# Kernel tuning notes

Hardware: AMD Instinct MI355X
Metric: run time of the kernel (lower is better)

The kernel has to match this reference:

```python
import jax, jax.numpy as jnp
import numpy as np

N = 500_000
H = 256
G = 4096
NUM_TIMESTEPS = 2


def setup_inputs() -> dict:
    key = jax.random.key(0)
    ks = jax.random.split(key, 12)
    s = 0.05
    x = jax.random.normal(ks[0], (N, H), dtype=jnp.float32)
    batch = jnp.sort(jax.random.randint(ks[1], (N,), 0, G, dtype=jnp.int64))
    return {
        "x": x,
        "gate_w1": jax.random.normal(ks[2], (H, H), dtype=jnp.float32) * s,
        "gate_b1": jax.random.normal(ks[3], (H,), dtype=jnp.float32) * s,
        "gate_w2": jax.random.normal(ks[4], (1, H), dtype=jnp.float32) * s,
        "gate_b2": jax.random.normal(ks[5], (1,), dtype=jnp.float32) * s,
        "gru_w_ih": jax.random.normal(ks[6], (3 * H, H), dtype=jnp.float32) * s,
        "gru_w_hh": jax.random.normal(ks[7], (3 * H, H), dtype=jnp.float32) * s,
        "gru_b_ih": jax.random.normal(ks[8], (3 * H,), dtype=jnp.float32) * s,
        "gru_b_hh": jax.random.normal(ks[9], (3 * H,), dtype=jnp.float32) * s,
        "batch": batch,
        "num_graphs": G,
    }


def _gru_cell(inp, h, w_ih, w_hh, b_ih, b_hh):
    # torch.nn.GRUCell semantics; gate order [r, z, n]
    gi = inp @ w_ih.T + b_ih
    gh = h @ w_hh.T + b_hh
    i_r, i_z, i_n = jnp.split(gi, 3, axis=-1)
    h_r, h_z, h_n = jnp.split(gh, 3, axis=-1)
    r = jax.nn.sigmoid(i_r + h_r)
    z = jax.nn.sigmoid(i_z + h_z)
    n = jnp.tanh(i_n + r * h_n)
    return (1.0 - z) * n + z * h


def reference(x, gate_w1, gate_b1, gate_w2, gate_b2,
              gru_w_ih, gru_w_hh, gru_b_ih, gru_b_hh,
              batch, num_graphs):
    counts = jax.ops.segment_sum(jnp.ones((x.shape[0],), x.dtype), batch,
                                 num_segments=num_graphs)
    denom = jnp.maximum(counts, 1.0)[:, None]  # empty graphs -> 0 mean

    def mean_pool(v):
        return jax.ops.segment_sum(v, batch, num_segments=num_graphs) / denom

    graph_repr = mean_pool(x)  # (G, H)
    for _ in range(NUM_TIMESTEPS):
        # gather per-node graph context (batch is sorted == node_to_graph)
        gate_input = x + graph_repr[batch]  # (N, H)
        hgate = jax.nn.relu(gate_input @ gate_w1.T + gate_b1)
        gate = jax.nn.sigmoid(hgate @ gate_w2.T + gate_b2)  # (N, 1)
        weighted_x = x * gate
        new_graph_repr = mean_pool(weighted_x)
        graph_repr = _gru_cell(new_graph_repr, graph_repr,
                               gru_w_ih, gru_w_hh, gru_b_ih, gru_b_hh)
        graph_repr = jax.nn.relu(graph_repr)
    return graph_repr
```

## Files before the change

### kernel.cpp

```cpp
#include <hip/hip_runtime.h>
#include <hip/hip_bf16.h>
#include <stdint.h>

#define H 256
#define G 4096
#define TK 32
#define TP0 128

typedef __attribute__((ext_vector_type(8))) short bf16x8;
typedef __attribute__((ext_vector_type(4))) float f32x4;

__device__ inline short f2bf(float f){
  union { float f; uint32_t u; } v; v.f = f;
  uint32_t r = (v.u + 0x7FFFu + ((v.u >> 16) & 1u)) >> 16;
  return (short)(uint16_t)r;
}
__device__ inline float bf2f(short s){
  union { float f; uint32_t u; } v; v.u = ((uint32_t)(uint16_t)s) << 16;
  return v.f;
}
__device__ inline uint32_t pk2(float lo, float hi){
  return (uint32_t)(uint16_t)f2bf(lo) | ((uint32_t)(uint16_t)f2bf(hi) << 16);
}
__device__ inline uint32_t pkfp8(float4 v){
  int u = __builtin_amdgcn_cvt_pk_fp8_f32(v.x, v.y, 0, false);
  u = __builtin_amdgcn_cvt_pk_fp8_f32(v.z, v.w, u, true);
  return (uint32_t)u;
}
__device__ inline float sigmoidf_(float x){ return 1.f / (1.f + __expf(-x)); }

__device__ inline void ldsbar(){
  asm volatile("s_waitcnt lgkmcnt(0)" ::: "memory");
  __builtin_amdgcn_s_barrier();
}

__global__ void conv_w(const float* __restrict__ w1, const float* __restrict__ wih,
                       const float* __restrict__ whh,
                       short* __restrict__ o1, short* __restrict__ oih, short* __restrict__ ohh,
                       uint8_t* __restrict__ w1q,
                       float* __restrict__ counts, float* __restrict__ pool){
  int i = blockIdx.x * 256 + threadIdx.x;
  if (i < H*H) o1[i] = f2bf(w1[i]);
  if (i < 3*H*H){ oih[i] = f2bf(wih[i]); ohh[i] = f2bf(whh[i]); }
  if (i < H*H/4){
    float4 v = *(const float4*)(w1 + (size_t)i*4);
    *(uint32_t*)(w1q + (size_t)i*4) = pkfp8(v);
  }
  if (i < G) counts[i] = 0.f;
  for (int j = i; j < G*H; j += 768*256) pool[j] = 0.f;
}

__global__ __launch_bounds__(512) __attribute__((amdgpu_waves_per_eu(2, 8)))
void k0_pool(const float* __restrict__ x, const int* __restrict__ batch,
             float* __restrict__ pool, float* __restrict__ counts,
             short* __restrict__ xbf, uint8_t* __restrict__ xq,
             float* __restrict__ sgate, int nNodes){
  __shared__ int   ng[TP0];
  __shared__ float Pacc[8][H];
  __shared__ float Cacc[8];
  __shared__ int   spanSh;

  const int t = threadIdx.x;
  const int base = blockIdx.x * TP0;
  const int c4 = (t & 63) * 4;
  const int r0 = (t >> 6) * 16;

  float4 v[16];
  #pragma unroll
  for (int i = 0; i < 16; ++i){
    int node = base + r0 + i;
    if (node < nNodes) v[i] = *(const float4*)(x + (size_t)node*H + c4);
    else v[i] = make_float4(0.f,0.f,0.f,0.f);
  }

  { int gi = blockIdx.x * 512 + t; if (gi < nNodes) sgate[gi] = 0.f; }

  if (t < TP0) ng[t] = (base + t < nNodes) ? batch[base + t] : -1;
  for (int u = t; u < 8*H; u += 512) ((float*)Pacc)[u] = 0.f;
  if (t < 8) Cacc[t] = 0.f;
  __syncthreads();

  if (t == 0){
    int lg = ng[0];
    if (base + TP0 <= nNodes) lg = ng[TP0-1];
    else { for (int i = TP0-1; i > 0; --i){ if (ng[i] >= 0){ lg = ng[i]; break; } } }
    spanSh = (ng[0] >= 0) ? (lg - ng[0]) : -1;
  }

  if (xbf){
    #pragma unroll
    for (int i = 0; i < 16; ++i){
      int node = base + r0 + i;
      if (node < nNodes){
        ushort4 o;
        o.x = (uint16_t)f2bf(v[i].x); o.y = (uint16_t)f2bf(v[i].y);
        o.z = (uint16_t)f2bf(v[i].z); o.w = (uint16_t)f2bf(v[i].w);
        *(ushort4*)(xbf + (size_t)node*H + c4) = o;
        *(uint32_t*)(xq + (size_t)node*H + c4) = pkfp8(v[i]);
      }
    }
  }
  __syncthreads();

  const int g0 = ng[0];
  const bool useLds = (spanSh >= 0) && (spanSh < 8);

  float ax=0.f, ay=0.f, az=0.f, aw=0.f;
  int cur = ng[r0];
  if (cur >= 0){
    #pragma unroll
    for (int i = 0; i < 16; ++i){
      int g = ng[r0 + i];
      if (g < 0) break;
      if (g != cur){
        if (useLds){
          atomicAdd(&Pacc[cur-g0][c4], ax);   atomicAdd(&Pacc[cur-g0][c4+1], ay);
          atomicAdd(&Pacc[cur-g0][c4+2], az); atomicAdd(&Pacc[cur-g0][c4+3], aw);
        } else {
          atomicAdd(&pool[(size_t)cur*H + c4], ax);   atomicAdd(&pool[(size_t)cur*H + c4+1], ay);
          atomicAdd(&pool[(size_t)cur*H + c4+2], az); atomicAdd(&pool[(size_t)cur*H + c4+3], aw);
        }
        ax=ay=az=aw=0.f; cur = g;
      }
      ax += v[i].x; ay += v[i].y; az += v[i].z; aw += v[i].w;
    }
    if (useLds){
      atomicAdd(&Pacc[cur-g0][c4], ax);   atomicAdd(&Pacc[cur-g0][c4+1], ay);
      atomicAdd(&Pacc[cur-g0][c4+2], az); atomicAdd(&Pacc[cur-g0][c4+3], aw);
    } else {
      atomicAdd(&pool[(size_t)cur*H + c4], ax);   atomicAdd(&pool[(size_t)cur*H + c4+1], ay);
      atomicAdd(&pool[(size_t)cur*H + c4+2], az); atomicAdd(&pool[(size_t)cur*H + c4+3], aw);
    }
  }
  if (t < TP0 && ng[t] >= 0){
    if (useLds) atomicAdd(&Cacc[ng[t]-g0], 1.f);
    else        atomicAdd(&counts[ng[t]], 1.f);
  }
  __syncthreads();

  if (useLds){
    int nr = spanSh + 1;
    for (int u = t; u < nr*H; u += 512){
      int r = u >> 8, c = u & 255;
      float vv = Pacc[r][c];
      if (vv != 0.f) atomicAdd(&pool[(size_t)(g0+r)*H + c], vv);
    }
    if (t < nr && Cacc[t] != 0.f) atomicAdd(&counts[g0 + t], Cacc[t]);
  }
}

__global__ void k0b_div(const float* __restrict__ pool, const float* __restrict__ counts,
                        float* __restrict__ repr, float* __restrict__ pool_mut){
  size_t i = (size_t)blockIdx.x * 256 + threadIdx.x;
  int g = (int)(i >> 8);
  repr[i] = pool[i] / fmaxf(counts[g], 1.f);
  pool_mut[i] = 0.f;
}

__global__ __launch_bounds__(256) void kT_hg(const float* __restrict__ repr,
    const short* __restrict__ w1bf, const float* __restrict__ b1,
    uint32_t* __restrict__ hgp){
  __shared__ short Ar[16][H + 8];
  const int t    = threadIdx.x;
  const int wid  = t >> 6;
  const int lane = t & 63;
  const int l15  = lane & 15;
  const int l4   = lane >> 4;
  const int g0   = blockIdx.x * 16;

  for (int u = t; u < 16*32; u += 256){
    int row = u >> 5, cg = u & 31;
    int c0 = cg * 8;
    const float4* rp = (const float4*)(repr + (size_t)(g0+row)*H + c0);
    float4 r0 = rp[0], r1 = rp[1];
    bf16x8 o;
    o[0]=f2bf(r0.x); o[1]=f2bf(r0.y); o[2]=f2bf(r0.z); o[3]=f2bf(r0.w);
    o[4]=f2bf(r1.x); o[5]=f2bf(r1.y); o[6]=f2bf(r1.z); o[7]=f2bf(r1.w);
    *(bf16x8*)(&Ar[row][c0]) = o;
  }
  __syncthreads();

  f32x4 acc[4];
  #pragma unroll
  for (int i = 0; i < 4; ++i) acc[i] = (f32x4){0.f,0.f,0.f,0.f};
  #pragma unroll
  for (int kc = 0; kc < 8; ++kc){
    bf16x8 a = *(bf16x8*)(&Ar[l15][kc*32 + l4*8]);
    #pragma unroll
    for (int nt = 0; nt < 4; ++nt){
      int col = wid*64 + nt*16 + l15;
      bf16x8 b = *(const bf16x8*)(w1bf + (size_t)col*H + kc*32 + l4*8);
      acc[nt] = __builtin_amdgcn_mfma_f32_16x16x32_bf16(a, b, acc[nt], 0, 0, 0);
    }
  }
  const float b1v0 = b1[wid*64 + l15];
  const float b1v1 = b1[wid*64 + 16 + l15];
  const float b1v2 = b1[wid*64 + 32 + l15];
  const float b1v3 = b1[wid*64 + 48 + l15];
  #pragma unroll
  for (int j = 0; j < 4; ++j){
    int row = l4*4 + j;
    hgp[(size_t)(g0+row)*128 + wid*32 + l15]      = pk2(acc[0][j]+b1v0, acc[1][j]+b1v1);
    hgp[(size_t)(g0+row)*128 + wid*32 + 16 + l15] = pk2(acc[2][j]+b1v2, acc[3][j]+b1v3);
  }
}

__global__ __launch_bounds__(256) __attribute__((amdgpu_waves_per_eu(4, 6)))
void k1a_fp8(
    const uint8_t* __restrict__ xq, const int* __restrict__ batch,
    const uint32_t* __restrict__ hgp, const uint8_t* __restrict__ w1q,
    const float* __restrict__ w2, float* __restrict__ sgate,
    int nNodes, int nTiles, int nChains){

  __shared__ uint8_t Ain[2][TK][H + 16];
  __shared__ int     ngS[2][TK];

  const int t    = threadIdx.x;
  const int wid  = t >> 6;
  const int lane = t & 63;
  const int l15  = lane & 15;
  const int l4   = lane >> 4;

  const int ch    = blockIdx.x >= nChains;
  const int chain = ch ? blockIdx.x - nChains : blockIdx.x;
  const int colB  = ch*128 + wid*32;
  const int hgcol = ch*64 + wid*16 + l15;

  const int tile0 = (int)(((long long)chain * nTiles) / nChains);
  const int tile1 = (int)(((long long)(chain+1) * nTiles) / nChains);
  if (tile0 >= tile1) return;

  long Bf0[8], Bf1[8];
  {
    const uint8_t* wp0 = w1q + (size_t)(colB + l15)*H + l4*8;
    #pragma unroll
    for (int kc = 0; kc < 8; ++kc){
      Bf0[kc] = *(const long*)(wp0 + kc*32);
      Bf1[kc] = *(const long*)(wp0 + 16*H + kc*32);
    }
  }
  const float w2v0 = w2[colB + l15];
  const float w2v1 = w2[colB + 16 + l15];

  const int srow  = t >> 4;
  const int scolB = (t & 15) * 16;
  uint4 xv0, xv1;
  int ngv = -1;

  auto issueT = [&](int tile){
    int base = tile * TK;
    int n0 = base + srow, n1 = n0 + 16;
    xv0 = (n0 < nNodes) ? *(const uint4*)(xq + (size_t)n0*H + scolB) : make_uint4(0,0,0,0);
    xv1 = (n1 < nNodes) ? *(const uint4*)(xq + (size_t)n1*H + scolB) : make_uint4(0,0,0,0);
    if (t < TK){
      int node = base + t;
      ngv = (node < nNodes) ? batch[node] : -1;
    }
  };
  auto stageT = [&](int buf){
    *(uint4*)(&Ain[buf][srow][scolB])      = xv0;
    *(uint4*)(&Ain[buf][srow + 16][scolB]) = xv1;
    if (t < TK) ngS[buf][t] = ngv;
  };

  issueT(tile0);
  stageT(0);
  if (tile0 + 1 < tile1) issueT(tile0 + 1);

  int cur = 0;
  for (int tile = tile0; tile < tile1; ++tile, cur ^= 1){
    ldsbar();

    int gr[2][4];
    uint32_t hvp[2][4];
    #pragma unroll
    for (int r = 0; r < 2; ++r)
      #pragma unroll
      for (int j = 0; j < 4; ++j){
        int g = ngS[cur][r*16 + l4*4 + j];
        gr[r][j] = g;
        hvp[r][j] = (g >= 0) ? hgp[(size_t)g*128 + hgcol] : 0u;
      }

    f32x4 acc0[2], acc1[2];
    #pragma unroll
    for (int r = 0; r < 2; ++r){ acc0[r] = (f32x4){0.f,0.f,0.f,0.f}; acc1[r] = (f32x4){0.f,0.f,0.f,0.f}; }
    #pragma unroll
    for (int kc = 0; kc < 8; ++kc){
      #pragma unroll
      for (int r = 0; r < 2; ++r){
        long a = *(const long*)(&Ain[cur][r*16 + l15][kc*32 + l4*8]);
        acc0[r] = __builtin_amdgcn_mfma_f32_16x16x32_fp8_fp8(a, Bf0[kc], acc0[r], 0, 0, 0);
        acc1[r] = __builtin_amdgcn_mfma_f32_16x16x32_fp8_fp8(a, Bf1[kc], acc1[r], 0, 0, 0);
      }
    }

    if (tile + 1 < tile1){
      stageT(cur ^ 1);
      if (tile + 2 < tile1) issueT(tile + 2);
    }

    float p[2][4];
    #pragma unroll
    for (int r = 0; r < 2; ++r)
      #pragma unroll
      for (int j = 0; j < 4; ++j){
        float h0 = fmaxf(acc0[r][j] + bf2f((short)(uint16_t)(hvp[r][j] & 0xFFFFu)), 0.f);
        float h1 = fmaxf(acc1[r][j] + bf2f((short)(uint16_t)(hvp[r][j] >> 16)), 0.f);
        p[r][j] = w2v0*h0 + w2v1*h1;
      }
    #pragma unroll
    for (int off = 1; off < 16; off <<= 1){
      #pragma unroll
      for (int r = 0; r < 2; ++r)
        #pragma unroll
        for (int j = 0; j < 4; ++j) p[r][j] += __shfl_xor(p[r][j], off);
    }
    if (l15 == 0){
      int base = tile * TK;
      #pragma unroll
      for (int r = 0; r < 2; ++r)
        #pragma unroll
        for (int j = 0; j < 4; ++j){
          if (gr[r][j] >= 0)
            atomicAdd(&sgate[base + r*16 + l4*4 + j], p[r][j]);
        }
    }
  }
}

template<bool BF>
__global__ __launch_bounds__(512) __attribute__((amdgpu_waves_per_eu(2, 8)))
void k1b_pool(
    const float* __restrict__ xf32, const short* __restrict__ xbf,
    const int* __restrict__ batch, float* __restrict__ sgate,
    const float* __restrict__ b2p, float* __restrict__ pool, int nNodes){

  __shared__ int   ng[TP0];
  __shared__ float gs[TP0];
  __shared__ float Pacc[8][H];
  __shared__ int   spanSh;

  const int t = threadIdx.x;
  const int base = blockIdx.x * TP0;
  const int c4 = (t & 63) * 4;
  const int r0 = (t >> 6) * 16;

  ushort4 u[16];
  float4  vf[16];
  #pragma unroll
  for (int i = 0; i < 16; ++i){
    int node = base + r0 + i;
    if constexpr (BF){
      u[i] = (node < nNodes) ? *(const ushort4*)(xbf + (size_t)node*H + c4)
                             : make_ushort4(0,0,0,0);
    } else {
      vf[i] = (node < nNodes) ? *(const float4*)(xf32 + (size_t)node*H + c4)
                              : make_float4(0.f,0.f,0.f,0.f);
    }
  }

  const float b2v = b2p[0];
  if (t < TP0){
    int node = base + t;
    if (node < nNodes){
      ng[t] = batch[node];
      gs[t] = sigmoidf_(sgate[node] + b2v);
      sgate[node] = 0.f;
    } else { ng[t] = -1; gs[t] = 0.f; }
  }
  for (int w = t; w < 8*H; w += 512) ((float*)Pacc)[w] = 0.f;
  __syncthreads();

  if (t == 0){
    int lg = ng[0];
    if (base + TP0 <= nNodes) lg = ng[TP0-1];
    else { for (int i = TP0-1; i > 0; --i){ if (ng[i] >= 0){ lg = ng[i]; break; } } }
    spanSh = (ng[0] >= 0) ? (lg - ng[0]) : -1;
  }
  __syncthreads();

  const int g0 = ng[0];
  const bool useLds = (spanSh >= 0) && (spanSh < 8);

  float ax=0.f, ay=0.f, az=0.f, aw=0.f;
  int cur = ng[r0];
  if (cur >= 0){
    #pragma unroll
    for (int i = 0; i < 16; ++i){
      int g = ng[r0 + i];
      if (g < 0) break;
      if (g != cur){
        if (useLds){
          atomicAdd(&Pacc[cur-g0][c4], ax);   atomicAdd(&Pacc[cur-g0][c4+1], ay);
          atomicAdd(&Pacc[cur-g0][c4+2], az); atomicAdd(&Pacc[cur-g0][c4+3], aw);
        } else {
          atomicAdd(&pool[(size_t)cur*H + c4], ax);   atomicAdd(&pool[(size_t)cur*H + c4+1], ay);
          atomicAdd(&pool[(size_t)cur*H + c4+2], az); atomicAdd(&pool[(size_t)cur*H + c4+3], aw);
        }
        ax=ay=az=aw=0.f; cur = g;
      }
      float gv = gs[r0 + i];
      if constexpr (BF){
        ax += gv * bf2f((short)u[i].x); ay += gv * bf2f((short)u[i].y);
        az += gv * bf2f((short)u[i].z); aw += gv * bf2f((short)u[i].w);
      } else {
        ax += gv * bf2f(f2bf(vf[i].x)); ay += gv * bf2f(f2bf(vf[i].y));
        az += gv * bf2f(f2bf(vf[i].z)); aw += gv * bf2f(f2bf(vf[i].w));
      }
    }
    if (useLds){
      atomicAdd(&Pacc[cur-g0][c4], ax);   atomicAdd(&Pacc[cur-g0][c4+1], ay);
      atomicAdd(&Pacc[cur-g0][c4+2], az); atomicAdd(&Pacc[cur-g0][c4+3], aw);
    } else {
      atomicAdd(&pool[(size_t)cur*H + c4], ax);   atomicAdd(&pool[(size_t)cur*H + c4+1], ay);
      atomicAdd(&pool[(size_t)cur*H + c4+2], az); atomicAdd(&pool[(size_t)cur*H + c4+3], aw);
    }
  }
  __syncthreads();

  if (useLds){
    int nr = spanSh + 1;
    for (int w = t; w < nr*H; w += 512){
      int r = w >> 8, c = w & 255;
      float vv = Pacc[r][c];
      if (vv != 0.f) atomicAdd(&pool[(size_t)(g0+r)*H + c], vv);
    }
  }
}

__global__ __launch_bounds__(256) __attribute__((amdgpu_waves_per_eu(3, 4)))
void k1a_gate_f32(
    const float* __restrict__ xf32, const int* __restrict__ batch,
    const uint32_t* __restrict__ hgp, const short* __restrict__ w1bf,
    const float* __restrict__ w2, float* __restrict__ sgate,
    int nNodes, int nTiles, int nChains){

  __shared__ short Ain[2][TK][H + 8];
  __shared__ int   ngS[2][TK];

  const int t    = threadIdx.x;
  const int wid  = t >> 6;
  const int lane = t & 63;
  const int l15  = lane & 15;
  const int l4   = lane >> 4;

  const int ch    = blockIdx.x >= nChains;
  const int chain = ch ? blockIdx.x - nChains : blockIdx.x;
  const int colB  = ch*128 + wid*32;
  const int hgcol = ch*64 + wid*16 + l15;

  const int tile0 = (int)(((long long)chain * nTiles) / nChains);
  const int tile1 = (int)(((long long)(chain+1) * nTiles) / nChains);
  if (tile0 >= tile1) return;

  bf16x8 Bf0[8], Bf1[8];
  {
    const short* wp0 = w1bf + (size_t)(colB + l15)*H + l4*8;
    #pragma unroll
    for (int kc = 0; kc < 8; ++kc){
      Bf0[kc] = *(const bf16x8*)(wp0 + kc*32);
      Bf1[kc] = *(const bf16x8*)(wp0 + 16*H + kc*32);
    }
  }
  const float w2v0 = w2[colB + l15];
  const float w2v1 = w2[colB + 16 + l15];

  const int srow = t >> 5;
  const int scol = (t & 31) * 8;
  float4 xf[4][2];
  int ngv = -1;

  auto issueT = [&](int tile){
    int base = tile * TK;
    #pragma unroll
    for (int q = 0; q < 4; ++q){
      int node = base + srow + q*8;
      if (node < nNodes){
        const float4* xp = (const float4*)(xf32 + (size_t)node*H + scol);
        xf[q][0] = xp[0]; xf[q][1] = xp[1];
      } else { xf[q][0] = make_float4(0.f,0.f,0.f,0.f); xf[q][1] = make_float4(0.f,0.f,0.f,0.f); }
    }
    if (t < TK){
      int node = base + t;
      ngv = (node < nNodes) ? batch[node] : -1;
    }
  };
  auto stageT = [&](int buf){
    #pragma unroll
    for (int q = 0; q < 4; ++q){
      bf16x8 o;
      float4 a = xf[q][0], c = xf[q][1];
      o[0]=f2bf(a.x); o[1]=f2bf(a.y); o[2]=f2bf(a.z); o[3]=f2bf(a.w);
      o[4]=f2bf(c.x); o[5]=f2bf(c.y); o[6]=f2bf(c.z); o[7]=f2bf(c.w);
      *(bf16x8*)(&Ain[buf][srow + q*8][scol]) = o;
    }
    if (t < TK) ngS[buf][t] = ngv;
  };

  issueT(tile0);
  stageT(0);
  if (tile0 + 1 < tile1) issueT(tile0 + 1);

  int cur = 0;
  for (int tile = tile0; tile < tile1; ++tile, cur ^= 1){
    ldsbar();

    int gr[2][4];
    uint32_t hvp[2][4];
    #pragma unroll
    for (int r = 0; r < 2; ++r)
      #pragma unroll
      for (int j = 0; j < 4; ++j){
        int g = ngS[cur][r*16 + l4*4 + j];
        gr[r][j] = g;
        hvp[r][j] = (g >= 0) ? hgp[(size_t)g*128 + hgcol] : 0u;
      }

    f32x4 acc0[2], acc1[2];
    #pragma unroll
    for (int r = 0; r < 2; ++r){ acc0[r] = (f32x4){0.f,0.f,0.f,0.f}; acc1[r] = (f32x4){0.f,0.f,0.f,0.f}; }
    #pragma unroll
    for (int kc = 0; kc < 8; ++kc){
      #pragma unroll
      for (int r = 0; r < 2; ++r){
        bf16x8 a = *(bf16x8*)(&Ain[cur][r*16 + l15][kc*32 + l4*8]);
        acc0[r] = __builtin_amdgcn_mfma_f32_16x16x32_bf16(a, Bf0[kc], acc0[r], 0, 0, 0);
        acc1[r] = __builtin_amdgcn_mfma_f32_16x16x32_bf16(a, Bf1[kc], acc1[r], 0, 0, 0);
      }
    }

    if (tile + 1 < tile1){
      stageT(cur ^ 1);
      if (tile + 2 < tile1) issueT(tile + 2);
    }

    float p[2][4];
    #pragma unroll
    for (int r = 0; r < 2; ++r)
      #pragma unroll
      for (int j = 0; j < 4; ++j){
        float h0 = fmaxf(acc0[r][j] + bf2f((short)(uint16_t)(hvp[r][j] & 0xFFFFu)), 0.f);
        float h1 = fmaxf(acc1[r][j] + bf2f((short)(uint16_t)(hvp[r][j] >> 16)), 0.f);
        p[r][j] = w2v0*h0 + w2v1*h1;
      }
    #pragma unroll
    for (int off = 1; off < 16; off <<= 1){
      #pragma unroll
      for (int r = 0; r < 2; ++r)
        #pragma unroll
        for (int j = 0; j < 4; ++j) p[r][j] += __shfl_xor(p[r][j], off);
    }
    if (l15 == 0){
      int base = tile * TK;
      #pragma unroll
      for (int r = 0; r < 2; ++r)
        #pragma unroll
        for (int j = 0; j < 4; ++j){
          if (gr[r][j] >= 0)
            atomicAdd(&sgate[base + r*16 + l4*4 + j], p[r][j]);
        }
    }
  }
}

__global__ __launch_bounds__(256) void k2_gru(float* __restrict__ pool,
    const float* __restrict__ counts, const float* __restrict__ repr_in,
    const short* __restrict__ wihbf, const short* __restrict__ whhbf,
    const float* __restrict__ bih, const float* __restrict__ bhh,
    float* __restrict__ repr_out,
    const short* __restrict__ w1bf, const float* __restrict__ b1,
    uint32_t* __restrict__ hgp, int doHg){

  __shared__ short Anew[16][H + 8];
  __shared__ short Aold[16][H + 8];
  __shared__ float hold[16][H];
  __shared__ float srz[16][2*H];
  __shared__ float sni[16][H];
  __shared__ float snh[16][H];

  const int t    = threadIdx.x;
  const int wid  = t >> 6;
  const int lane = t & 63;
  const int l15  = lane & 15;
  const int l4   = lane >> 4;
  const int g0   = blockIdx.x * 16;

  for (int u = t; u < 16*H; u += 256){
    int row = u >> 8, c = u & 255;
    int g = g0 + row;
    float cnt = fmaxf(counts[g], 1.f);
    float rin = repr_in[(size_t)g*H + c];
    float nr  = pool[(size_t)g*H + c] / cnt;
    pool[(size_t)g*H + c] = 0.f;
    Anew[row][c] = f2bf(nr);
    Aold[row][c] = f2bf(rin);
    hold[row][c] = rin;
  }
  __syncthreads();

  f32x4 ai[12], ah[12];
  #pragma unroll
  for (int i = 0; i < 12; ++i){ ai[i] = (f32x4){0.f,0.f,0.f,0.f}; ah[i] = (f32x4){0.f,0.f,0.f,0.f}; }

  for (int kc = 0; kc < 8; ++kc){
    bf16x8 an = *(bf16x8*)(&Anew[l15][kc*32 + l4*8]);
    bf16x8 ao = *(bf16x8*)(&Aold[l15][kc*32 + l4*8]);
    #pragma unroll
    for (int nt = 0; nt < 12; ++nt){
      int n = wid*192 + nt*16 + l15;
      bf16x8 bi = *(const bf16x8*)(wihbf + (size_t)n*H + kc*32 + l4*8);
      bf16x8 bh = *(const bf16x8*)(whhbf + (size_t)n*H + kc*32 + l4*8);
      ai[nt] = __builtin_amdgcn_mfma_f32_16x16x32_bf16(an, bi, ai[nt], 0, 0, 0);
      ah[nt] = __builtin_amdgcn_mfma_f32_16x16x32_bf16(ao, bh, ah[nt], 0, 0, 0);
    }
  }

  #pragma unroll
  for (int nt = 0; nt < 12; ++nt){
    int n = wid*192 + nt*16 + l15;
    float bi = bih[n], bh = bhh[n];
    #pragma unroll
    for (int r = 0; r < 4; ++r){
      int row = l4*4 + r;
      float si = ai[nt][r] + bi;
      float sh = ah[nt][r] + bh;
      if (n < 2*H) srz[row][n] = si + sh;
      else { sni[row][n - 2*H] = si; snh[row][n - 2*H] = sh; }
    }
  }
  __syncthreads();

  for (int u = t; u < 16*H; u += 256){
    int row = u >> 8, c = u & 255;
    float rr = sigmoidf_(srz[row][c]);
    float zz = sigmoidf_(srz[row][H + c]);
    float nn = tanhf(sni[row][c] + rr * snh[row][c]);
    float hv = (1.f - zz) * nn + zz * hold[row][c];
    float out = fmaxf(hv, 0.f);
    repr_out[(size_t)(g0 + row)*H + c] = out;
    Anew[row][c] = f2bf(out);
  }

  if (doHg){
    __syncthreads();
    f32x4 acc[4];
    #pragma unroll
    for (int i = 0; i < 4; ++i) acc[i] = (f32x4){0.f,0.f,0.f,0.f};
    #pragma unroll
    for (int kc = 0; kc < 8; ++kc){
      bf16x8 a = *(bf16x8*)(&Anew[l15][kc*32 + l4*8]);
      #pragma unroll
      for (int nt = 0; nt < 4; ++nt){
        int col = wid*64 + nt*16 + l15;
        bf16x8 b = *(const bf16x8*)(w1bf + (size_t)col*H + kc*32 + l4*8);
        acc[nt] = __builtin_amdgcn_mfma_f32_16x16x32_bf16(a, b, acc[nt], 0, 0, 0);
      }
    }
    const float b1v0 = b1[wid*64 + l15];
    const float b1v1 = b1[wid*64 + 16 + l15];
    const float b1v2 = b1[wid*64 + 32 + l15];
    const float b1v3 = b1[wid*64 + 48 + l15];
    #pragma unroll
    for (int j = 0; j < 4; ++j){
      int row = l4*4 + j;
      hgp[(size_t)(g0+row)*128 + wid*32 + l15]      = pk2(acc[0][j]+b1v0, acc[1][j]+b1v1);
      hgp[(size_t)(g0+row)*128 + wid*32 + 16 + l15] = pk2(acc[2][j]+b1v2, acc[3][j]+b1v3);
    }
  }
}

extern "C" void kernel_launch(void* const* d_in, const int* in_sizes, int n_in,
                              void* d_out, int out_size, void* d_ws, size_t ws_size,
                              hipStream_t stream){
  const float* x    = (const float*)d_in[0];
  const float* w1   = (const float*)d_in[1];
  const float* b1   = (const float*)d_in[2];
  const float* w2   = (const float*)d_in[3];
  const float* b2   = (const float*)d_in[4];
  const float* wih  = (const float*)d_in[5];
  const float* whh  = (const float*)d_in[6];
  const float* bih  = (const float*)d_in[7];
  const float* bhh  = (const float*)d_in[8];
  const int*   batch= (const int*)d_in[9];
  const int N = in_sizes[9];

  char* ws = (char*)d_ws;
  short* w1bf   = (short*)(ws + 0);
  short* wihbf  = (short*)(ws + (1u<<17));
  short* whhbf  = (short*)(ws + (1u<<19));
  float* counts = (float*)(ws + 917504);
  uint8_t* w1q  = (uint8_t*)(ws + 933888);
  float* pool   = (float*)(ws + (1u<<20));
  float* repr   = (float*)(ws + (1u<<20) + (1u<<22));
  float* sgate  = (float*)(ws + (9u<<20));
  uint32_t* hgp = (uint32_t*)(ws + (12u<<20));
  float* outp   = (float*)d_out;

  const size_t XBF_OFF = (size_t)16u << 20;
  const size_t XQ_OFF  = XBF_OFF + ((size_t)272u << 20);
  const bool useXbf = ws_size >= XQ_OFF + (size_t)N * H;
  short*   xbf = useXbf ? (short*)(ws + XBF_OFF) : nullptr;
  uint8_t* xq  = useXbf ? (uint8_t*)(ws + XQ_OFF) : nullptr;

  const int nTiles  = (N + TK - 1) / TK;
  const int nChains = useXbf ? 640 : 512;
  const int nBlk1a  = nChains * 2;
  const int nBlkP   = (N + TP0 - 1) / TP0;

  conv_w<<<768, 256, 0, stream>>>(w1, wih, whh, w1bf, wihbf, whhbf, w1q, counts, pool);
  k0_pool<<<nBlkP, 512, 0, stream>>>(x, batch, pool, counts, xbf, xq, sgate, N);
  k0b_div<<<G*H/256, 256, 0, stream>>>(pool, counts, repr, pool);
  kT_hg<<<G/16, 256, 0, stream>>>(repr, w1bf, b1, hgp);

  for (int ts = 0; ts < 2; ++ts){
    if (useXbf){
      k1a_fp8<<<nBlk1a, 256, 0, stream>>>(xq, batch, hgp, w1q, w2, sgate, N, nTiles, nChains);
      k1b_pool<true><<<nBlkP, 512, 0, stream>>>(x, xbf, batch, sgate, b2, pool, N);
    } else {
      k1a_gate_f32<<<nBlk1a, 256, 0, stream>>>(x, batch, hgp, w1bf, w2, sgate, N, nTiles, nChains);
      k1b_pool<false><<<nBlkP, 512, 0, stream>>>(x, xbf, batch, sgate, b2, pool, N);
    }
    k2_gru<<<G/16, 256, 0, stream>>>(pool, counts, repr, wihbf, whhbf, bih, bhh,
                                     (ts == 0) ? repr : outp,
                                     w1bf, b1, hgp, (ts == 0) ? 1 : 0);
  }
}
```

Baseline: 699.0 us.

## Compute all gate columns per block in k1a and fuse mean-divide into hg kernel

The fp8 gate kernel now has each block cover all 256 hidden columns (64 per wave, in two passes) instead of splitting columns across two block halves. Each x tile is then loaded and staged only once rather than twice, at the cost of doubled B-fragment registers and a lower waves-per-EU target. Separately, the mean-divide and pool-zeroing kernel is folded into the hg-projection kernel, removing one launch and one pass over the pool and repr buffers.

New measurement: 668.1 us. 4.4% less time.

```diff
diff --git a/kernel.cpp b/kernel.cpp
--- a/kernel.cpp
+++ b/kernel.cpp
@@ -149,15 +149,8 @@
   }
 }
 
-__global__ void k0b_div(const float* __restrict__ pool, const float* __restrict__ counts,
-                        float* __restrict__ repr, float* __restrict__ pool_mut){
-  size_t i = (size_t)blockIdx.x * 256 + threadIdx.x;
-  int g = (int)(i >> 8);
-  repr[i] = pool[i] / fmaxf(counts[g], 1.f);
-  pool_mut[i] = 0.f;
-}
-
-__global__ __launch_bounds__(256) void kT_hg(const float* __restrict__ repr,
+__global__ __launch_bounds__(256) void kT2(float* __restrict__ pool,
+    const float* __restrict__ counts, float* __restrict__ repr,
     const short* __restrict__ w1bf, const float* __restrict__ b1,
     uint32_t* __restrict__ hgp){
   __shared__ short Ar[16][H + 8];
@@ -171,11 +164,19 @@
   for (int u = t; u < 16*32; u += 256){
     int row = u >> 5, cg = u & 31;
     int c0 = cg * 8;
-    const float4* rp = (const float4*)(repr + (size_t)(g0+row)*H + c0);
-    float4 r0 = rp[0], r1 = rp[1];
+    int g = g0 + row;
+    float cnt = fmaxf(counts[g], 1.f);
+    float4* pp = (float4*)(pool + (size_t)g*H + c0);
+    float4 p0 = pp[0], p1 = pp[1];
+    p0.x/=cnt; p0.y/=cnt; p0.z/=cnt; p0.w/=cnt;
+    p1.x/=cnt; p1.y/=cnt; p1.z/=cnt; p1.w/=cnt;
+    float4* rp = (float4*)(repr + (size_t)g*H + c0);
+    rp[0] = p0; rp[1] = p1;
+    pp[0] = make_float4(0.f,0.f,0.f,0.f);
+    pp[1] = make_float4(0.f,0.f,0.f,0.f);
     bf16x8 o;
-    o[0]=f2bf(r0.x); o[1]=f2bf(r0.y); o[2]=f2bf(r0.z); o[3]=f2bf(r0.w);
-    o[4]=f2bf(r1.x); o[5]=f2bf(r1.y); o[6]=f2bf(r1.z); o[7]=f2bf(r1.w);
+    o[0]=f2bf(p0.x); o[1]=f2bf(p0.y); o[2]=f2bf(p0.z); o[3]=f2bf(p0.w);
+    o[4]=f2bf(p1.x); o[5]=f2bf(p1.y); o[6]=f2bf(p1.z); o[7]=f2bf(p1.w);
     *(bf16x8*)(&Ar[row][c0]) = o;
   }
   __syncthreads();
@@ -205,12 +206,12 @@
   }
 }
 
-__global__ __launch_bounds__(256) __attribute__((amdgpu_waves_per_eu(4, 6)))
+__global__ __launch_bounds__(256) __attribute__((amdgpu_waves_per_eu(3, 4)))
 void k1a_fp8(
     const uint8_t* __restrict__ xq, const int* __restrict__ batch,
     const uint32_t* __restrict__ hgp, const uint8_t* __restrict__ w1q,
     const float* __restrict__ w2, float* __restrict__ sgate,
-    int nNodes, int nTiles, int nChains){
+    int nNodes, int nTiles, int nBlk){
 
   __shared__ uint8_t Ain[2][TK][H + 16];
   __shared__ int     ngS[2][TK];
@@ -220,27 +221,27 @@
   const int lane = t & 63;
   const int l15  = lane & 15;
   const int l4   = lane >> 4;
-
-  const int ch    = blockIdx.x >= nChains;
-  const int chain = ch ? blockIdx.x - nChains : blockIdx.x;
-  const int colB  = ch*128 + wid*32;
-  const int hgcol = ch*64 + wid*16 + l15;
-
-  const int tile0 = (int)(((long long)chain * nTiles) / nChains);
-  const int tile1 = (int)(((long long)(chain+1) * nTiles) / nChains);
+  const int colB = wid*64;
+
+  const int tile0 = (int)(((long long)blockIdx.x * nTiles) / nBlk);
+  const int tile1 = (int)(((long long)(blockIdx.x+1) * nTiles) / nBlk);
   if (tile0 >= tile1) return;
 
-  long Bf0[8], Bf1[8];
+  long BfA0[8], BfA1[8], BfB0[8], BfB1[8];
   {
-    const uint8_t* wp0 = w1q + (size_t)(colB + l15)*H + l4*8;
+    const uint8_t* wp = w1q + (size_t)(colB + l15)*H + l4*8;
     #pragma unroll
     for (int kc = 0; kc < 8; ++kc){
-      Bf0[kc] = *(const long*)(wp0 + kc*32);
-      Bf1[kc] = *(const long*)(wp0 + 16*H + kc*32);
-    }
-  }
-  const float w2v0 = w2[colB + l15];
-  const float w2v1 = w2[colB + 16 + l15];
+      BfA0[kc] = *(const long*)(wp + kc*32);
+      BfA1[kc] = *(const long*)(wp + 16*H + kc*32);
+      BfB0[kc] = *(const long*)(wp + 32*H + kc*32);
+      BfB1[kc] = *(const long*)(wp + 48*H + kc*32);
+    }
+  }
+  const float w2A0 = w2[colB + l15];
+  const float w2A1 = w2[colB + 16 + l15];
+  const float w2B0 = w2[colB + 32 + l15];
+  const float w2B1 = w2[colB + 48 + l15];
 
   const int srow  = t >> 4;
   const int scolB = (t & 15) * 16;
@@ -271,15 +272,13 @@
   for (int tile = tile0; tile < tile1; ++tile, cur ^= 1){
     ldsbar();
 
-    int gr[2][4];
     uint32_t hvp[2][4];
     #pragma unroll
     for (int r = 0; r < 2; ++r)
       #pragma unroll
       for (int j = 0; j < 4; ++j){
         int g = ngS[cur][r*16 + l4*4 + j];
-        gr[r][j] = g;
-        hvp[r][j] = (g >= 0) ? hgp[(size_t)g*128 + hgcol] : 0u;
+        hvp[r][j] = (g >= 0) ? hgp[(size_t)g*128 + wid*32 + l15] : 0u;
       }
 
     f32x4 acc0[2], acc1[2];
@@ -290,8 +289,8 @@
       #pragma unroll
       for (int r = 0; r < 2; ++r){
         long a = *(const long*)(&Ain[cur][r*16 + l15][kc*32 + l4*8]);
-        acc0[r] = __builtin_amdgcn_mfma_f32_16x16x32_fp8_fp8(a, Bf0[kc], acc0[r], 0, 0, 0);
-        acc1[r] = __builtin_amdgcn_mfma_f32_16x16x32_fp8_fp8(a, Bf1[kc], acc1[r], 0, 0, 0);
+        acc0[r] = __builtin_amdgcn_mfma_f32_16x16x32_fp8_fp8(a, BfA0[kc], acc0[r], 0, 0, 0);
+        acc1[r] = __builtin_amdgcn_mfma_f32_16x16x32_fp8_fp8(a, BfA1[kc], acc1[r], 0, 0, 0);
       }
     }
 
@@ -307,8 +306,36 @@
       for (int j = 0; j < 4; ++j){
         float h0 = fmaxf(acc0[r][j] + bf2f((short)(uint16_t)(hvp[r][j] & 0xFFFFu)), 0.f);
         float h1 = fmaxf(acc1[r][j] + bf2f((short)(uint16_t)(hvp[r][j] >> 16)), 0.f);
-        p[r][j] = w2v0*h0 + w2v1*h1;
-      }
+        p[r][j] = w2A0*h0 + w2A1*h1;
+      }
+
+    #pragma unroll
+    for (int r = 0; r < 2; ++r)
+      #pragma unroll
+      for (int j = 0; j < 4; ++j){
+        int g = ngS[cur][r*16 + l4*4 + j];
+        hvp[r][j] = (g >= 0) ? hgp[(size_t)g*128 + wid*32 + 16 + l15] : 0u;
+      }
+    #pragma unroll
+    for (int r = 0; r < 2; ++r){ acc0[r] = (f32x4){0.f,0.f,0.f,0.f}; acc1[r] = (f32x4){0.f,0.f,0.f,0.f}; }
+    #pragma unroll
+    for (int kc = 0; kc < 8; ++kc){
+      #pragma unroll
+      for (int r = 0; r < 2; ++r){
+        long a = *(const long*)(&Ain[cur][r*16 + l15][kc*32 + l4*8]);
+        acc0[r] = __builtin_amdgcn_mfma_f32_16x16x32_fp8_fp8(a, BfB0[kc], acc0[r], 0, 0, 0);
+        acc1[r] = __builtin_amdgcn_mfma_f32_16x16x32_fp8_fp8(a, BfB1[kc], acc1[r], 0, 0, 0);
+      }
+    }
+    #pragma unroll
+    for (int r = 0; r < 2; ++r)
+      #pragma unroll
+      for (int j = 0; j < 4; ++j){
+        float h0 = fmaxf(acc0[r][j] + bf2f((short)(uint16_t)(hvp[r][j] & 0xFFFFu)), 0.f);
+        float h1 = fmaxf(acc1[r][j] + bf2f((short)(uint16_t)(hvp[r][j] >> 16)), 0.f);
+        p[r][j] += w2B0*h0 + w2B1*h1;
+      }
+
     #pragma unroll
     for (int off = 1; off < 16; off <<= 1){
       #pragma unroll
@@ -322,8 +349,9 @@
       for (int r = 0; r < 2; ++r)
         #pragma unroll
         for (int j = 0; j < 4; ++j){
-          if (gr[r][j] >= 0)
-            atomicAdd(&sgate[base + r*16 + l4*4 + j], p[r][j]);
+          int idx = r*16 + l4*4 + j;
+          if (ngS[cur][idx] >= 0)
+            atomicAdd(&sgate[base + idx], p[r][j]);
         }
     }
   }
@@ -704,21 +732,20 @@
   uint8_t* xq  = useXbf ? (uint8_t*)(ws + XQ_OFF) : nullptr;
 
   const int nTiles  = (N + TK - 1) / TK;
-  const int nChains = useXbf ? 640 : 512;
-  const int nBlk1a  = nChains * 2;
+  const int nBlk1a  = 1024;
+  const int nChainsF= 512;
   const int nBlkP   = (N + TP0 - 1) / TP0;
 
   conv_w<<<768, 256, 0, stream>>>(w1, wih, whh, w1bf, wihbf, whhbf, w1q, counts, pool);
   k0_pool<<<nBlkP, 512, 0, stream>>>(x, batch, pool, counts, xbf, xq, sgate, N);
-  k0b_div<<<G*H/256, 256, 0, stream>>>(pool, counts, repr, pool);
-  kT_hg<<<G/16, 256, 0, stream>>>(repr, w1bf, b1, hgp);
+  kT2<<<G/16, 256, 0, stream>>>(pool, counts, repr, w1bf, b1, hgp);
 
   for (int ts = 0; ts < 2; ++ts){
     if (useXbf){
-      k1a_fp8<<<nBlk1a, 256, 0, stream>>>(xq, batch, hgp, w1q, w2, sgate, N, nTiles, nChains);
+      k1a_fp8<<<nBlk1a, 256, 0, stream>>>(xq, batch, hgp, w1q, w2, sgate, N, nTiles, nBlk1a);
       k1b_pool<true><<<nBlkP, 512, 0, stream>>>(x, xbf, batch, sgate, b2, pool, N);
     } else {
-      k1a_gate_f32<<<nBlk1a, 256, 0, stream>>>(x, batch, hgp, w1bf, w2, sgate, N, nTiles, nChains);
+      k1a_gate_f32<<<nChainsF*2, 256, 0, stream>>>(x, batch, hgp, w1bf, w2, sgate, N, nTiles, nChainsF);
       k1b_pool<false><<<nBlkP, 512, 0, stream>>>(x, xbf, batch, sgate, b2, pool, N);
     }
     k2_gru<<<G/16, 256, 0, stream>>>(pool, counts, repr, wihbf, whhbf, bih, bhh,
```
